# Performance work log

Measured on AMD Instinct MI355X. Metric: run time of the kernel, lower is better.

The kernel has to match this reference:

```python
import jax, jax.numpy as jnp
import numpy as np

STYLE_STRENGTH = 0.5
EPS = 1e-8


def _whiten(f):
    # f: [C, H, W] -> ZCA-whitened feature (zero mean, identity covariance)
    C = f.shape[0]
    x = f.reshape(C, -1)
    mu = x.mean(axis=1, keepdims=True)
    xc = x - mu
    cov = (xc @ xc.T) / (x.shape[1] - 1)          # [C, C]
    evals, evecs = jnp.linalg.eigh(cov)
    evals = jnp.maximum(evals, EPS)
    Wm = (evecs * (evals ** -0.5)) @ evecs.T
    return (Wm @ xc).reshape(f.shape)


def _color(f, style):
    # recolor whitened f with the covariance/mean of style. f, style: [C, H, W]
    C = f.shape[0]
    x = f.reshape(C, -1)
    s = style.reshape(C, -1)
    smu = s.mean(axis=1, keepdims=True)
    sc = s - smu
    cov = (sc @ sc.T) / (s.shape[1] - 1)
    evals, evecs = jnp.linalg.eigh(cov)
    evals = jnp.maximum(evals, EPS)
    Cm = (evecs * (evals ** 0.5)) @ evecs.T
    return (Cm @ x + smu).reshape(f.shape)


def _extract_patches3(f):
    # f: [B, C, H, W] -> [B, P, C, 3, 3], P = (H-2)*(W-2), stride 1, no padding
    B, C, H, W = f.shape
    nh, nw = H - 2, W - 2
    shifts = [f[:, :, i:i + nh, j:j + nw] for i in range(3) for j in range(3)]
    p = jnp.stack(shifts, axis=-1)                      # [B, C, nh, nw, 9]
    p = p.reshape(B, C, nh * nw, 9).transpose(0, 2, 1, 3)
    return p.reshape(B, nh * nw, C, 3, 3)


def _conv_valid(x, k):
    # x: [C, Hp, Wp], k: [O, C, kh, kw] -> [O, Hp-kh+1, Wp-kw+1]
    return jax.lax.conv_general_dilated(
        x[None], k, window_strides=(1, 1), padding='VALID',
        dimension_numbers=('NCHW', 'OIHW', 'NCHW'))[0]


def _deconv_norm(H, W, k, dtype):
    # overlap counts of k x k patches at stride 1 with centered crop (pad=(k-1)//2)
    th = jnp.arange(1, H + 1)
    tw = jnp.arange(1, W + 1)
    rh = (jnp.minimum(th, k - 1) - jnp.maximum(0, th - (H - 1)) + 1).astype(dtype)
    rw = (jnp.minimum(tw, k - 1) - jnp.maximum(0, tw - (W - 1)) + 1).astype(dtype)
    return rh[:, None] * rw[None, :]                    # [H, W]


def setup_inputs() -> dict:
    key = jax.random.key(0)
    kc, ks = jax.random.split(key)
    B, C, H, W = 4, 512, 64, 64
    return {
        'content_feature': jax.random.normal(kc, (B, C, H, W), dtype=jnp.float32),
        'style_feature': jax.random.normal(ks, (B, C, H, W), dtype=jnp.float32),
        'patch_size': 3,
        'patch_stride': 1,
    }


def reference(content_feature, style_feature, patch_size, patch_stride):
    B, C, H, W = content_feature.shape
    pad = (patch_size - 1) // 2

    # whitening of content and style features (per-sample ZCA)
    nc = jax.vmap(_whiten)(content_feature)
    ns = jax.vmap(_whiten)(style_feature)

    # style patches as conv kernels: [B, P, C, 3, 3]
    kern = _extract_patches3(ns)
    knorm = jnp.sqrt(jnp.sum(kern * kern, axis=(2, 3, 4), keepdims=True))
    kern_n = kern / knorm

    # cosine-similarity matching conv: [B, P, H, W]
    ncp = jnp.pad(nc, ((0, 0), (0, 0), (pad, pad), (pad, pad)))
    score = jax.vmap(_conv_valid)(ncp, kern_n)

    # hard argmax one-hot over patch dim
    P = kern.shape[1]
    idx = jnp.argmax(score, axis=1)                     # [B, H, W]
    onehot = jax.nn.one_hot(idx, P, dtype=score.dtype).transpose(0, 3, 1, 2)

    # transpose-conv reassembly == conv with flipped, channel-swapped kernels
    oh_pad = jnp.pad(onehot, ((0, 0), (0, 0), (pad, pad), (pad, pad)))
    kern_t = jnp.flip(kern, axis=(-2, -1)).transpose(0, 2, 1, 3, 4)  # [B, C, P, 3, 3]
    deconv = jax.vmap(_conv_valid)(oh_pad, kern_t)      # [B, C, H, W]

    reassembled = deconv / _deconv_norm(H, W, patch_size, deconv.dtype)[None, None]

    # recolor with style statistics, blend with content
    stylized = jax.vmap(_color)(reassembled, style_feature)
    return (1.0 - STYLE_STRENGTH) * content_feature + STYLE_STRENGTH * stylized
```

## Files before the change

kernel.cpp:

```cpp
#include <hip/hip_runtime.h>
#include <stdint.h>


#define C_   512
#define H_   64
#define W_   64
#define HW_  4096
#define P_   3844
#define PW_  62
#define NIT_ 10

static const long CHW_ = (long)C_ * HW_;
static const long CC_  = (long)C_ * C_;

typedef _Float16 f16x8 __attribute__((ext_vector_type(8)));
typedef float    f32x16 __attribute__((ext_vector_type(16)));

enum { GM_COV = 0, GM_NST = 1, GM_PLAIN = 2, GM_SCALE_RCP = 3, GM_NSMUL = 4, GM_NSMUL_F = 5, GM_COLOR = 6 };

template<int MODE, bool TB>
__global__ __launch_bounds__(256)
void gemm_k(const float* __restrict__ A, const float* __restrict__ Bm, float* __restrict__ Cm_,
            const float* __restrict__ sarr, const float* __restrict__ ex1, const float* __restrict__ ex2,
            int M, int N, int K, long sA, long sB, long sC, long sE1, float cscale)
{
    int z = blockIdx.z;
    const float* Ab; const float* Bb; float* Cb;
    float fs = 1.0f;
    if (MODE == GM_NSMUL || MODE == GM_NSMUL_F) {
        if (z < 8) {
            Ab = A   + (long)z * CC_;
            Bb = ex1 + (long)z * CC_;
            if (MODE == GM_NSMUL_F) fs = sqrtf(sarr[z]);
        } else {
            Ab = ex1 + (long)(z - 8) * CC_;
            Bb = Bm  + (long)(z - 8) * CC_;
            if (MODE == GM_NSMUL_F) fs = rsqrtf(sarr[z - 8]);
        }
        Cb = Cm_ + (long)z * CC_;
    } else {
        Ab = A   + (long)z * sA;
        Bb = Bm  + (long)z * sB;
        Cb = Cm_ + (long)z * sC;
        if (MODE == GM_SCALE_RCP) fs = 1.0f / sarr[z];
    }

    __shared__ float As[16][64];
    __shared__ float Bs[16][64];

    int tid = threadIdx.x;
    int tx = tid & 15, ty = tid >> 4;
    int i0 = blockIdx.x * 64;
    int j0 = blockIdx.y * 64;

    int lr = tid >> 2;
    int lk = (tid & 3) << 2;

    float acc[4][4] = {};

    for (int k0 = 0; k0 < K; k0 += 16) {
        float4 va = *(const float4*)(Ab + (long)(i0 + lr) * K + (k0 + lk));
        As[lk + 0][lr] = va.x; As[lk + 1][lr] = va.y; As[lk + 2][lr] = va.z; As[lk + 3][lr] = va.w;
        if (TB) {
            float4 vb = *(const float4*)(Bb + (long)(j0 + lr) * K + (k0 + lk));
            Bs[lk + 0][lr] = vb.x; Bs[lk + 1][lr] = vb.y; Bs[lk + 2][lr] = vb.z; Bs[lk + 3][lr] = vb.w;
        } else {
            int kr = tid >> 4, jc = (tid & 15) << 2;
            float4 vb = *(const float4*)(Bb + (long)(k0 + kr) * N + (j0 + jc));
            *(float4*)&Bs[kr][jc] = vb;
        }
        __syncthreads();
        #pragma unroll
        for (int k = 0; k < 16; ++k) {
            float4 av = *(const float4*)&As[k][ty * 4];
            float4 bv = *(const float4*)&Bs[k][tx * 4];
            acc[0][0] += av.x * bv.x; acc[0][1] += av.x * bv.y; acc[0][2] += av.x * bv.z; acc[0][3] += av.x * bv.w;
            acc[1][0] += av.y * bv.x; acc[1][1] += av.y * bv.y; acc[1][2] += av.y * bv.z; acc[1][3] += av.y * bv.w;
            acc[2][0] += av.z * bv.x; acc[2][1] += av.z * bv.y; acc[2][2] += av.z * bv.z; acc[2][3] += av.z * bv.w;
            acc[3][0] += av.w * bv.x; acc[3][1] += av.w * bv.y; acc[3][2] += av.w * bv.z; acc[3][3] += av.w * bv.w;
        }
        __syncthreads();
    }

    #pragma unroll
    for (int u = 0; u < 4; ++u) {
        int row  = i0 + ty * 4 + u;
        int col0 = j0 + tx * 4;
        float o[4];
        if (MODE == GM_COLOR) {
            const float* cv = ex1 + (long)z * sE1 + (long)row * N + col0;
            float mu = ex2[z * C_ + row];
            #pragma unroll
            for (int v = 0; v < 4; ++v) o[v] = 0.5f * cv[v] + 0.5f * (acc[u][v] + mu);
        } else {
            #pragma unroll
            for (int v = 0; v < 4; ++v) {
                if (MODE == GM_COV)      o[v] = acc[u][v] * cscale;
                else if (MODE == GM_NST) o[v] = (row == col0 + v ? 1.5f : 0.0f) - 0.5f * acc[u][v];
                else                     o[v] = acc[u][v] * fs;
            }
        }
        *(float4*)&Cb[(long)row * N + col0] = make_float4(o[0], o[1], o[2], o[3]);
    }
}

__global__ __launch_bounds__(256)
void k_center(const float* __restrict__ content, const float* __restrict__ style,
              float* __restrict__ xc, float* __restrict__ means)
{
    int bz = blockIdx.x;
    int z = bz >> 9, c = bz & 511;
    const float* src = (z < 4) ? (content + ((long)z * C_ + c) * HW_)
                               : (style   + ((long)(z - 4) * C_ + c) * HW_);
    float* dst = xc + (long)bz * HW_;
    int tid = threadIdx.x;
    float s = 0.f;
    for (int k = tid; k < HW_; k += 256) s += src[k];
    __shared__ float red[4];
    #pragma unroll
    for (int m = 32; m >= 1; m >>= 1) s += __shfl_down(s, m);
    if ((tid & 63) == 0) red[tid >> 6] = s;
    __syncthreads();
    float mean = (red[0] + red[1] + red[2] + red[3]) * (1.0f / HW_);
    for (int k = tid; k < HW_; k += 256) dst[k] = src[k] - mean;
    if (tid == 0) means[bz] = mean;
}

__global__ void k_infnorm(const float* __restrict__ cov, float* __restrict__ snorm)
{
    int z = blockIdx.x; int tid = threadIdx.x;
    const float* Mz = cov + (long)z * CC_;
    for (int r = tid; r < C_; r += 256) {
        const float4* row = (const float4*)(Mz + (long)r * C_);
        float s = 0.f;
        for (int k = 0; k < C_ / 4; ++k) {
            float4 v = row[k];
            s += fabsf(v.x) + fabsf(v.y) + fabsf(v.z) + fabsf(v.w);
        }
        atomicMax((unsigned*)&snorm[z], __float_as_uint(s));
    }
}

__global__ void k_nsinit(const float* __restrict__ cov, const float* __restrict__ snorm,
                         float* __restrict__ T, float* __restrict__ Z1)
{
    long i = (long)blockIdx.x * 256 + threadIdx.x;
    int z = (int)(i >> 18);
    long rc = i & (CC_ - 1);
    int row = (int)(rc >> 9), col = (int)(rc & 511);
    float v = -0.5f * cov[i] / snorm[z];
    if (row == col) v += 1.5f;
    T[i] = v;
    Z1[i] = v;
}

__global__ void k_q(const float* __restrict__ nsw, float* __restrict__ q)
{
    int b = blockIdx.x, y = blockIdx.y * 4 + threadIdx.y, x = threadIdx.x;
    const float* base = nsw + (long)b * CHW_ + y * W_ + x;
    float s = 0.f;
    for (int c = 0; c < C_; ++c) { float v = base[(long)c * HW_]; s += v * v; }
    q[(long)b * HW_ + y * W_ + x] = s;
}

__global__ void k_rkn(const float* __restrict__ q, float* __restrict__ rkn)
{
    int b = blockIdx.x;
    const float* qb = q + (long)b * HW_;
    for (int p = threadIdx.x; p < P_; p += 256) {
        int pu = p / PW_, pv = p % PW_;
        float s = 0.f;
        #pragma unroll
        for (int i = 0; i < 3; ++i)
            #pragma unroll
            for (int j = 0; j < 3; ++j)
                s += qb[(pu + i) * W_ + pv + j];
        rkn[b * P_ + p] = rsqrtf(fmaxf(s, 1e-20f));
    }
}

#define SC_CH 16
__global__ __launch_bounds__(256)
void k_score(const float* __restrict__ nc, const float* __restrict__ nsw,
             const float* __restrict__ rkn, unsigned long long* __restrict__ packed)
{
    int b  = blockIdx.z;
    int p0 = blockIdx.x * 256;
    int y0 = blockIdx.y;
    const float* ncb = nc  + (long)b * CHW_;
    const float* nsb = nsw + (long)b * CHW_;

    __shared__ __align__(16) _Float16 sA[2][2][3][66][8];
    __shared__ __align__(16) _Float16 sB[2][2][8][64][8];

    int tid  = threadIdx.x;
    int w    = tid >> 6;
    int lane = tid & 63;
    int l31  = lane & 31;
    int h    = lane >> 5;

    int pu0 = p0 / PW_;
    int pw0 = p0 + w * 64;

    int pn0 = pw0 + l31;
    int pn1 = pw0 + 32 + l31;
    int q0 = pn0 < P_ - 1 ? pn0 : P_ - 1;
    int q1 = pn1 < P_ - 1 ? pn1 : P_ - 1;
    int brow0 = q0 / PW_ - pu0, bcol0 = q0 % PW_;
    int brow1 = q1 / PW_ - pu0, bcol1 = q1 % PW_;

    f32x16 acc00 = {}, acc01 = {}, acc10 = {}, acc11 = {};

    for (int c0 = 0; c0 < C_; c0 += SC_CH) {
        for (int idx = tid; idx < 2 * 3 * 66; idx += 256) {
            int x = idx % 66; int gr = idx / 66;
            int r = gr % 3, g = gr / 3;
            int gy = y0 - 1 + r, gx = x - 1;
            bool ok = ((unsigned)gy < 64u) && ((unsigned)gx < 64u);
            const float* src = ncb + (long)(c0 + g * 8) * HW_ + gy * W_ + gx;
            f16x8 hi8, lo8;
            #pragma unroll
            for (int e = 0; e < 8; ++e) {
                float v = ok ? src[(long)e * HW_] : 0.f;
                _Float16 hi = (_Float16)v;
                hi8[e] = hi;
                lo8[e] = (_Float16)(v - (float)hi);
            }
            *(f16x8*)&sA[0][g][r][x][0] = hi8;
            *(f16x8*)&sA[1][g][r][x][0] = lo8;
        }
        for (int idx = tid; idx < 2 * 8 * 64; idx += 256) {
            int x = idx & 63; int gr = idx >> 6;
            int r = gr & 7, g = gr >> 3;
            int gy = pu0 + r;
            bool ok = gy < 64;
            const float* src = nsb + (long)(c0 + g * 8) * HW_ + gy * W_ + x;
            f16x8 hi8, lo8;
            #pragma unroll
            for (int e = 0; e < 8; ++e) {
                float v = ok ? src[(long)e * HW_] : 0.f;
                _Float16 hi = (_Float16)v;
                hi8[e] = hi;
                lo8[e] = (_Float16)(v - (float)hi);
            }
            *(f16x8*)&sB[0][g][r][x][0] = hi8;
            *(f16x8*)&sB[1][g][r][x][0] = lo8;
        }
        __syncthreads();

        #pragma unroll
        for (int i = 0; i < 3; ++i) {
            #pragma unroll
            for (int j = 0; j < 3; ++j) {
                f16x8 a0h = *(const f16x8*)&sA[0][h][i][l31 + j][0];
                f16x8 a0l = *(const f16x8*)&sA[1][h][i][l31 + j][0];
                f16x8 a1h = *(const f16x8*)&sA[0][h][i][32 + l31 + j][0];
                f16x8 a1l = *(const f16x8*)&sA[1][h][i][32 + l31 + j][0];
                f16x8 b0h = *(const f16x8*)&sB[0][h][brow0 + i][bcol0 + j][0];
                f16x8 b0l = *(const f16x8*)&sB[1][h][brow0 + i][bcol0 + j][0];
                f16x8 b1h = *(const f16x8*)&sB[0][h][brow1 + i][bcol1 + j][0];
                f16x8 b1l = *(const f16x8*)&sB[1][h][brow1 + i][bcol1 + j][0];

                acc00 = __builtin_amdgcn_mfma_f32_32x32x16_f16(a0l, b0h, acc00, 0, 0, 0);
                acc00 = __builtin_amdgcn_mfma_f32_32x32x16_f16(a0h, b0l, acc00, 0, 0, 0);
                acc00 = __builtin_amdgcn_mfma_f32_32x32x16_f16(a0h, b0h, acc00, 0, 0, 0);

                acc01 = __builtin_amdgcn_mfma_f32_32x32x16_f16(a0l, b1h, acc01, 0, 0, 0);
                acc01 = __builtin_amdgcn_mfma_f32_32x32x16_f16(a0h, b1l, acc01, 0, 0, 0);
                acc01 = __builtin_amdgcn_mfma_f32_32x32x16_f16(a0h, b1h, acc01, 0, 0, 0);

                acc10 = __builtin_amdgcn_mfma_f32_32x32x16_f16(a1l, b0h, acc10, 0, 0, 0);
                acc10 = __builtin_amdgcn_mfma_f32_32x32x16_f16(a1h, b0l, acc10, 0, 0, 0);
                acc10 = __builtin_amdgcn_mfma_f32_32x32x16_f16(a1h, b0h, acc10, 0, 0, 0);

                acc11 = __builtin_amdgcn_mfma_f32_32x32x16_f16(a1l, b1h, acc11, 0, 0, 0);
                acc11 = __builtin_amdgcn_mfma_f32_32x32x16_f16(a1h, b1l, acc11, 0, 0, 0);
                acc11 = __builtin_amdgcn_mfma_f32_32x32x16_f16(a1h, b1h, acc11, 0, 0, 0);
            }
        }
        __syncthreads();
    }

    bool v0 = pn0 < P_, v1 = pn1 < P_;
    float rk0 = v0 ? rkn[b * P_ + pn0] : 0.f;
    float rk1 = v1 ? rkn[b * P_ + pn1] : 0.f;

    #pragma unroll
    for (int mt = 0; mt < 2; ++mt) {
        const f32x16& A0 = mt ? acc10 : acc00;
        const f32x16& A1 = mt ? acc11 : acc01;
        #pragma unroll
        for (int r = 0; r < 16; ++r) {
            float s0 = v0 ? A0[r] * rk0 : -3.0e38f;
            float s1 = v1 ? A1[r] * rk1 : -3.0e38f;
            float best = s0; int bp = pn0;
            if (s1 > best) { best = s1; bp = pn1; }
            #pragma unroll
            for (int m = 1; m <= 16; m <<= 1) {
                float ob = __shfl_xor(best, m);
                int   op = __shfl_xor(bp, m);
                if (ob > best || (ob == best && op < bp)) { best = ob; bp = op; }
            }
            if (l31 == 0 && best > -2.9e38f) {
                int mr = (r & 3) + 8 * (r >> 2) + 4 * h;
                int px = mt * 32 + mr;
                unsigned ub = __float_as_uint(best);
                ub = (ub & 0x80000000u) ? ~ub : (ub | 0x80000000u);
                unsigned long long enc = ((unsigned long long)ub << 32) | (unsigned)(0xFFFFFFFFu - (unsigned)bp);
                atomicMax(&packed[(long)b * HW_ + y0 * W_ + px], enc);
            }
        }
    }
}

__global__ __launch_bounds__(256)
void k_reasm(const unsigned long long* __restrict__ packed, const float* __restrict__ nsw,
             float* __restrict__ reasm)
{
    int b = blockIdx.x, y = blockIdx.y;
    int x = threadIdx.x, tc = threadIdx.y;
    const float* nsb = nsw + (long)b * CHW_;
    int soff[9]; float msk[9];
    #pragma unroll
    for (int dy = -1; dy <= 1; ++dy) {
        #pragma unroll
        for (int dx = -1; dx <= 1; ++dx) {
            int k = (dy + 1) * 3 + (dx + 1);
            int u = y + dy, v = x + dx;
            if ((unsigned)u < 64u && (unsigned)v < 64u) {
                unsigned long long e = packed[(long)b * HW_ + u * W_ + v];
                int p = (int)(0xFFFFFFFFu - (unsigned)(e & 0xFFFFFFFFull));
                int pu = p / PW_, pv = p - pu * PW_;
                soff[k] = (pu + (1 - dy)) * W_ + (pv + (1 - dx));
                msk[k] = 1.f;
            } else { soff[k] = 0; msk[k] = 0.f; }
        }
    }
    int rh = (y == 0 || y == 63) ? 2 : 3;
    int rw = (x == 0 || x == 63) ? 2 : 3;
    float inv = 1.f / (float)(rh * rw);
    for (int c = tc; c < C_; c += 4) {
        const float* cb = nsb + (long)c * HW_;
        float s = 0.f;
        #pragma unroll
        for (int k = 0; k < 9; ++k) s += msk[k] * cb[soff[k]];
        reasm[((long)b * C_ + c) * HW_ + y * W_ + x] = s * inv;
    }
}

extern "C" void kernel_launch(void* const* d_in, const int* in_sizes, int n_in,
                              void* d_out, int out_size, void* d_ws, size_t ws_size,
                              hipStream_t stream)
{
    const float* content = (const float*)d_in[0];
    const float* style   = (const float*)d_in[1];
    float* out = (float*)d_out;
    float* ws  = (float*)d_ws;

    float* XC    = ws;
    float* NC    = XC    + 8 * CHW_;
    float* SLABA = NC    + 8 * CHW_;
    float* SLABB = SLABA + 16 * CC_;
    float* TBUF  = SLABB + 16 * CC_;
    float* MEANS = TBUF  + 8 * CC_;
    float* SNORM = MEANS + 4096;
    float* Q     = SNORM + 16;
    float* RKN   = Q     + 16384;
    unsigned long long* PACKED = (unsigned long long*)(RKN + 15392);

    float* COV   = SLABB;
    float* REASM = XC;

    hipMemsetAsync(SNORM, 0, 16 * sizeof(float), stream);
    hipMemsetAsync(PACKED, 0, (size_t)4 * HW_ * 8, stream);

    k_center<<<dim3(4096), dim3(256), 0, stream>>>(content, style, XC, MEANS);

    gemm_k<GM_COV, true><<<dim3(8, 8, 8), dim3(256), 0, stream>>>(
        XC, XC, COV, nullptr, nullptr, nullptr, 512, 512, 4096, CHW_, CHW_, CC_, 0, 1.0f / 4095.0f);

    k_infnorm<<<dim3(8), dim3(256), 0, stream>>>(COV, SNORM);
    k_nsinit<<<dim3(8192), dim3(256), 0, stream>>>(COV, SNORM, TBUF, SLABA + 8 * CC_);
    gemm_k<GM_SCALE_RCP, false><<<dim3(8, 8, 8), dim3(256), 0, stream>>>(
        COV, TBUF, SLABA, SNORM, nullptr, nullptr, 512, 512, 512, CC_, CC_, CC_, 0, 0.f);

    float* curS = SLABA; float* outS = SLABB;
    for (int it = 2; it <= NIT_; ++it) {
        gemm_k<GM_NST, false><<<dim3(8, 8, 8), dim3(256), 0, stream>>>(
            curS + 8 * CC_, curS, TBUF, nullptr, nullptr, nullptr, 512, 512, 512, CC_, CC_, CC_, 0, 0.f);
        if (it == NIT_)
            gemm_k<GM_NSMUL_F, false><<<dim3(8, 8, 16), dim3(256), 0, stream>>>(
                curS, curS + 8 * CC_, outS, SNORM, TBUF, nullptr, 512, 512, 512, 0, 0, 0, 0, 0.f);
        else
            gemm_k<GM_NSMUL, false><<<dim3(8, 8, 16), dim3(256), 0, stream>>>(
                curS, curS + 8 * CC_, outS, SNORM, TBUF, nullptr, 512, 512, 512, 0, 0, 0, 0, 0.f);
        float* t = curS; curS = outS; outS = t;
    }

    gemm_k<GM_PLAIN, false><<<dim3(8, 64, 8), dim3(256), 0, stream>>>(
        curS + 8 * CC_, XC, NC, nullptr, nullptr, nullptr, 512, 4096, 512, CC_, CHW_, CHW_, 0, 0.f);

    k_q<<<dim3(4, 16), dim3(64, 4), 0, stream>>>(NC + 4 * CHW_, Q);
    k_rkn<<<dim3(4), dim3(256), 0, stream>>>(Q, RKN);

    k_score<<<dim3(16, 64, 4), dim3(256), 0, stream>>>(NC, NC + 4 * CHW_, RKN, PACKED);

    k_reasm<<<dim3(4, 64), dim3(64, 4), 0, stream>>>(PACKED, NC + 4 * CHW_, REASM);

    gemm_k<GM_COLOR, false><<<dim3(8, 64, 4), dim3(256), 0, stream>>>(
        curS + 4 * CC_, REASM, out, nullptr, content, MEANS + 2048,
        512, 4096, 512, CC_, CHW_, CHW_, CHW_, 0.f);
}
```

Measured before the change: 3.656 ms.

## Move all GEMMs to split-fp16 MFMA with hi/lo operand storage

Replaces the scalar FP32 shared-memory GEMMs (covariance, Newton-Schulz iterations, whitening and coloring) with MFMA 32x32x16 fp16 kernels. Each operand is split into high and low fp16 parts, and three MFMAs per tile (hi*hi, hi*lo, lo*hi) approximate FP32 accuracy. Newton-Schulz matrices are now stored directly as hi/lo fp16 pairs, which halves the traffic for those intermediates and reorganises the workspace layout. The trade-off is extra conversion work on load and slightly reduced precision compared with true FP32.

```diff
diff --git a/kernel.cpp b/kernel.cpp
--- a/kernel.cpp
+++ b/kernel.cpp
@@ -16,91 +16,167 @@
 typedef _Float16 f16x8 __attribute__((ext_vector_type(8)));
 typedef float    f32x16 __attribute__((ext_vector_type(16)));
 
-enum { GM_COV = 0, GM_NST = 1, GM_PLAIN = 2, GM_SCALE_RCP = 3, GM_NSMUL = 4, GM_NSMUL_F = 5, GM_COLOR = 6 };
-
-template<int MODE, bool TB>
+#define SQ_NST  0
+#define SQ_MUL  1
+#define SQ_MULF 2
+#define RC_COV    0
+#define RC_WHITEN 1
+#define RC_COLOR  2
+
+template<int MODE>
 __global__ __launch_bounds__(256)
-void gemm_k(const float* __restrict__ A, const float* __restrict__ Bm, float* __restrict__ Cm_,
-            const float* __restrict__ sarr, const float* __restrict__ ex1, const float* __restrict__ ex2,
-            int M, int N, int K, long sA, long sB, long sC, long sE1, float cscale)
-{
+void gemm_sq(const _Float16* __restrict__ A1h, const _Float16* __restrict__ A1l,
+             const _Float16* __restrict__ B1h, const _Float16* __restrict__ B1l,
+             _Float16* __restrict__ D1h, _Float16* __restrict__ D1l,
+             const _Float16* __restrict__ A2h, const _Float16* __restrict__ A2l,
+             const _Float16* __restrict__ B2h, const _Float16* __restrict__ B2l,
+             _Float16* __restrict__ D2h, _Float16* __restrict__ D2l,
+             const float* __restrict__ sarr)
+{
+    int z = blockIdx.z; int zz = z & 7; bool sec = z >= 8;
+    const _Float16* Ah = (sec ? A2h : A1h) + (long)zz * CC_;
+    const _Float16* Al = (sec ? A2l : A1l) + (long)zz * CC_;
+    const _Float16* Bh = (sec ? B2h : B1h) + (long)zz * CC_;
+    const _Float16* Bl = (sec ? B2l : B1l) + (long)zz * CC_;
+    _Float16* Dh = (sec ? D2h : D1h) + (long)zz * CC_;
+    _Float16* Dl = (sec ? D2l : D1l) + (long)zz * CC_;
+    float scl = 1.0f;
+    if (MODE == SQ_MULF) scl = sec ? rsqrtf(sarr[zz]) : sqrtf(sarr[zz]);
+
+    __shared__ __align__(16) _Float16 sA[2][2][64][8];
+    __shared__ __align__(16) _Float16 sB[2][2][64][8];
+
+    int tid = threadIdx.x;
+    int w = tid >> 6, lane = tid & 63, l31 = lane & 31, h = lane >> 5;
+    int i0 = blockIdx.x * 64, j0 = blockIdx.y * 64;
+    int wm = (w >> 1) * 32, wn = (w & 1) * 32;
+
+    int spl = tid >> 7, sm = (tid >> 1) & 63, sh = tid & 1;
+    const _Float16* Asrc = spl ? Al : Ah;
+    const _Float16* Bsrc = spl ? Bl : Bh;
+
+    f32x16 acc = {};
+    for (int c0 = 0; c0 < 512; c0 += 16) {
+        *(f16x8*)&sA[spl][sh][sm][0] = *(const f16x8*)(Asrc + (long)(i0 + sm) * 512 + c0 + sh * 8);
+        *(f16x8*)&sB[spl][sh][sm][0] = *(const f16x8*)(Bsrc + (long)(j0 + sm) * 512 + c0 + sh * 8);
+        __syncthreads();
+        f16x8 ah = *(const f16x8*)&sA[0][h][wm + l31][0];
+        f16x8 al = *(const f16x8*)&sA[1][h][wm + l31][0];
+        f16x8 bh = *(const f16x8*)&sB[0][h][wn + l31][0];
+        f16x8 bl = *(const f16x8*)&sB[1][h][wn + l31][0];
+        acc = __builtin_amdgcn_mfma_f32_32x32x16_f16(al, bh, acc, 0, 0, 0);
+        acc = __builtin_amdgcn_mfma_f32_32x32x16_f16(ah, bl, acc, 0, 0, 0);
+        acc = __builtin_amdgcn_mfma_f32_32x32x16_f16(ah, bh, acc, 0, 0, 0);
+        __syncthreads();
+    }
+    #pragma unroll
+    for (int r = 0; r < 16; ++r) {
+        int row = i0 + wm + (r & 3) + 8 * (r >> 2) + 4 * h;
+        int col = j0 + wn + l31;
+        float v = acc[r];
+        if (MODE == SQ_NST) v = (row == col ? 1.5f : 0.0f) - 0.5f * v;
+        else                v *= scl;
+        _Float16 hi = (_Float16)v;
+        Dh[(long)row * 512 + col] = hi;
+        Dl[(long)row * 512 + col] = (_Float16)(v - (float)hi);
+    }
+}
+
+template<int MODE>
+__global__ __launch_bounds__(256)
+void gemm_rect(const _Float16* __restrict__ APh, const _Float16* __restrict__ APl,
+               const float* __restrict__ Asrc32, const float* __restrict__ Bsrc32,
+               float* __restrict__ Dout, const float* __restrict__ content,
+               const float* __restrict__ means)
+{
+    const int K = (MODE == RC_COV) ? 4096 : 512;
     int z = blockIdx.z;
-    const float* Ab; const float* Bb; float* Cb;
-    float fs = 1.0f;
-    if (MODE == GM_NSMUL || MODE == GM_NSMUL_F) {
-        if (z < 8) {
-            Ab = A   + (long)z * CC_;
-            Bb = ex1 + (long)z * CC_;
-            if (MODE == GM_NSMUL_F) fs = sqrtf(sarr[z]);
+    int tid = threadIdx.x;
+    int w = tid >> 6, lane = tid & 63, l31 = lane & 31, h = lane >> 5;
+    int i0 = blockIdx.x * 64, j0 = blockIdx.y * 128;
+    int wm = (w >> 1) * 32, wn = (w & 1) * 64;
+
+    __shared__ __align__(16) _Float16 sA[2][2][64][8];
+    __shared__ __align__(16) _Float16 sB[2][2][128][8];
+
+    const float* Bz = Bsrc32 + (long)z * CHW_;
+    int az = (MODE == RC_COLOR) ? z + 4 : z;
+
+    f32x16 acc0 = {}, acc1 = {};
+
+    for (int c0 = 0; c0 < K; c0 += 16) {
+        if (MODE == RC_COV) {
+            int m = tid >> 2, kq = tid & 3;
+            const float* a = Asrc32 + (long)z * CHW_ + (long)(i0 + m) * HW_ + c0 + kq * 4;
+            float4 va = *(const float4*)a;
+            _Float16 hi[4], lo[4];
+            float vv[4] = {va.x, va.y, va.z, va.w};
+            #pragma unroll
+            for (int e = 0; e < 4; ++e) { hi[e] = (_Float16)vv[e]; lo[e] = (_Float16)(vv[e] - (float)hi[e]); }
+            *(__attribute__((ext_vector_type(4))) _Float16*)&sA[0][kq >> 1][m][(kq & 1) * 4] =
+                *(__attribute__((ext_vector_type(4))) _Float16*)hi;
+            *(__attribute__((ext_vector_type(4))) _Float16*)&sA[1][kq >> 1][m][(kq & 1) * 4] =
+                *(__attribute__((ext_vector_type(4))) _Float16*)lo;
         } else {
-            Ab = ex1 + (long)(z - 8) * CC_;
-            Bb = Bm  + (long)(z - 8) * CC_;
-            if (MODE == GM_NSMUL_F) fs = rsqrtf(sarr[z - 8]);
-        }
-        Cb = Cm_ + (long)z * CC_;
-    } else {
-        Ab = A   + (long)z * sA;
-        Bb = Bm  + (long)z * sB;
-        Cb = Cm_ + (long)z * sC;
-        if (MODE == GM_SCALE_RCP) fs = 1.0f / sarr[z];
-    }
-
-    __shared__ float As[16][64];
-    __shared__ float Bs[16][64];
-
-    int tid = threadIdx.x;
-    int tx = tid & 15, ty = tid >> 4;
-    int i0 = blockIdx.x * 64;
-    int j0 = blockIdx.y * 64;
-
-    int lr = tid >> 2;
-    int lk = (tid & 3) << 2;
-
-    float acc[4][4] = {};
-
-    for (int k0 = 0; k0 < K; k0 += 16) {
-        float4 va = *(const float4*)(Ab + (long)(i0 + lr) * K + (k0 + lk));
-        As[lk + 0][lr] = va.x; As[lk + 1][lr] = va.y; As[lk + 2][lr] = va.z; As[lk + 3][lr] = va.w;
-        if (TB) {
-            float4 vb = *(const float4*)(Bb + (long)(j0 + lr) * K + (k0 + lk));
-            Bs[lk + 0][lr] = vb.x; Bs[lk + 1][lr] = vb.y; Bs[lk + 2][lr] = vb.z; Bs[lk + 3][lr] = vb.w;
+            int spl = tid >> 7, sm = (tid >> 1) & 63, sh = tid & 1;
+            const _Float16* a = (spl ? APl : APh) + (long)az * CC_ + (long)(i0 + sm) * 512 + c0 + sh * 8;
+            *(f16x8*)&sA[spl][sh][sm][0] = *(const f16x8*)a;
+        }
+        if (MODE == RC_COV) {
+            int n = tid >> 1, sh = tid & 1;
+            const float* b = Bz + (long)(j0 + n) * HW_ + c0 + sh * 8;
+            float4 v0 = *(const float4*)b, v1 = *(const float4*)(b + 4);
+            float vv[8] = {v0.x, v0.y, v0.z, v0.w, v1.x, v1.y, v1.z, v1.w};
+            f16x8 hi8, lo8;
+            #pragma unroll
+            for (int e = 0; e < 8; ++e) { _Float16 hh = (_Float16)vv[e]; hi8[e] = hh; lo8[e] = (_Float16)(vv[e] - (float)hh); }
+            *(f16x8*)&sB[0][sh][n][0] = hi8;
+            *(f16x8*)&sB[1][sh][n][0] = lo8;
         } else {
-            int kr = tid >> 4, jc = (tid & 15) << 2;
-            float4 vb = *(const float4*)(Bb + (long)(k0 + kr) * N + (j0 + jc));
-            *(float4*)&Bs[kr][jc] = vb;
+            int n = tid & 127, sh = tid >> 7;
+            const float* b = Bz + (long)(c0 + sh * 8) * HW_ + j0 + n;
+            f16x8 hi8, lo8;
+            #pragma unroll
+            for (int e = 0; e < 8; ++e) {
+                float v = b[(long)e * HW_];
+                _Float16 hh = (_Float16)v; hi8[e] = hh; lo8[e] = (_Float16)(v - (float)hh);
+            }
+            *(f16x8*)&sB[0][sh][n][0] = hi8;
+            *(f16x8*)&sB[1][sh][n][0] = lo8;
         }
         __syncthreads();
+        f16x8 ah = *(const f16x8*)&sA[0][h][wm + l31][0];
+        f16x8 al = *(const f16x8*)&sA[1][h][wm + l31][0];
+        f16x8 b0h = *(const f16x8*)&sB[0][h][wn + l31][0];
+        f16x8 b0l = *(const f16x8*)&sB[1][h][wn + l31][0];
+        f16x8 b1h = *(const f16x8*)&sB[0][h][wn + 32 + l31][0];
+        f16x8 b1l = *(const f16x8*)&sB[1][h][wn + 32 + l31][0];
+        acc0 = __builtin_amdgcn_mfma_f32_32x32x16_f16(al, b0h, acc0, 0, 0, 0);
+        acc0 = __builtin_amdgcn_mfma_f32_32x32x16_f16(ah, b0l, acc0, 0, 0, 0);
+        acc0 = __builtin_amdgcn_mfma_f32_32x32x16_f16(ah, b0h, acc0, 0, 0, 0);
+        acc1 = __builtin_amdgcn_mfma_f32_32x32x16_f16(al, b1h, acc1, 0, 0, 0);
+        acc1 = __builtin_amdgcn_mfma_f32_32x32x16_f16(ah, b1l, acc1, 0, 0, 0);
+        acc1 = __builtin_amdgcn_mfma_f32_32x32x16_f16(ah, b1h, acc1, 0, 0, 0);
+        __syncthreads();
+    }
+
+    #pragma unroll
+    for (int nt = 0; nt < 2; ++nt) {
+        const f32x16& A = nt ? acc1 : acc0;
         #pragma unroll
-        for (int k = 0; k < 16; ++k) {
-            float4 av = *(const float4*)&As[k][ty * 4];
-            float4 bv = *(const float4*)&Bs[k][tx * 4];
-            acc[0][0] += av.x * bv.x; acc[0][1] += av.x * bv.y; acc[0][2] += av.x * bv.z; acc[0][3] += av.x * bv.w;
-            acc[1][0] += av.y * bv.x; acc[1][1] += av.y * bv.y; acc[1][2] += av.y * bv.z; acc[1][3] += av.y * bv.w;
-            acc[2][0] += av.z * bv.x; acc[2][1] += av.z * bv.y; acc[2][2] += av.z * bv.z; acc[2][3] += av.z * bv.w;
-            acc[3][0] += av.w * bv.x; acc[3][1] += av.w * bv.y; acc[3][2] += av.w * bv.z; acc[3][3] += av.w * bv.w;
-        }
-        __syncthreads();
-    }
-
-    #pragma unroll
-    for (int u = 0; u < 4; ++u) {
-        int row  = i0 + ty * 4 + u;
-        int col0 = j0 + tx * 4;
-        float o[4];
-        if (MODE == GM_COLOR) {
-            const float* cv = ex1 + (long)z * sE1 + (long)row * N + col0;
-            float mu = ex2[z * C_ + row];
-            #pragma unroll
-            for (int v = 0; v < 4; ++v) o[v] = 0.5f * cv[v] + 0.5f * (acc[u][v] + mu);
-        } else {
-            #pragma unroll
-            for (int v = 0; v < 4; ++v) {
-                if (MODE == GM_COV)      o[v] = acc[u][v] * cscale;
-                else if (MODE == GM_NST) o[v] = (row == col0 + v ? 1.5f : 0.0f) - 0.5f * acc[u][v];
-                else                     o[v] = acc[u][v] * fs;
-            }
-        }
-        *(float4*)&Cb[(long)row * N + col0] = make_float4(o[0], o[1], o[2], o[3]);
+        for (int r = 0; r < 16; ++r) {
+            int row = i0 + wm + (r & 3) + 8 * (r >> 2) + 4 * h;
+            int col = j0 + wn + nt * 32 + l31;
+            if (MODE == RC_COV) {
+                Dout[(long)z * CC_ + (long)row * 512 + col] = A[r] * (1.0f / 4095.0f);
+            } else if (MODE == RC_WHITEN) {
+                Dout[(long)z * CHW_ + (long)row * HW_ + col] = A[r];
+            } else {
+                long idx = (long)z * CHW_ + (long)row * HW_ + col;
+                float mu = means[(z + 4) * C_ + row];
+                Dout[idx] = 0.5f * content[idx] + 0.5f * (A[r] + mu);
+            }
+        }
     }
 }
 
@@ -142,16 +218,19 @@
 }
 
 __global__ void k_nsinit(const float* __restrict__ cov, const float* __restrict__ snorm,
-                         float* __restrict__ T, float* __restrict__ Z1)
+                         _Float16* __restrict__ CVH, _Float16* __restrict__ CVL,
+                         _Float16* __restrict__ TH,  _Float16* __restrict__ TL,
+                         _Float16* __restrict__ ZH,  _Float16* __restrict__ ZL)
 {
     long i = (long)blockIdx.x * 256 + threadIdx.x;
     int z = (int)(i >> 18);
     long rc = i & (CC_ - 1);
     int row = (int)(rc >> 9), col = (int)(rc & 511);
-    float v = -0.5f * cov[i] / snorm[z];
-    if (row == col) v += 1.5f;
-    T[i] = v;
-    Z1[i] = v;
+    float cs = cov[i] / snorm[z];
+    float t = (row == col ? 1.5f : 0.0f) - 0.5f * cs;
+    _Float16 ch = (_Float16)cs; CVH[i] = ch; CVL[i] = (_Float16)(cs - (float)ch);
+    _Float16 th = (_Float16)t;  TH[i] = th;  TL[i] = (_Float16)(t - (float)th);
+    ZH[i] = th; ZL[i] = TL[i];
 }
 
 __global__ void k_q(const float* __restrict__ nsw, float* __restrict__ q)
@@ -355,20 +434,28 @@
     const float* content = (const float*)d_in[0];
     const float* style   = (const float*)d_in[1];
     float* out = (float*)d_out;
-    float* ws  = (float*)d_ws;
-
-    float* XC    = ws;
-    float* NC    = XC    + 8 * CHW_;
-    float* SLABA = NC    + 8 * CHW_;
-    float* SLABB = SLABA + 16 * CC_;
-    float* TBUF  = SLABB + 16 * CC_;
-    float* MEANS = TBUF  + 8 * CC_;
-    float* SNORM = MEANS + 4096;
-    float* Q     = SNORM + 16;
-    float* RKN   = Q     + 16384;
-    unsigned long long* PACKED = (unsigned long long*)(RKN + 15392);
-
-    float* COV   = SLABB;
+
+    char* base = (char*)d_ws;
+    float* XC = (float*)base;
+    float* NC = XC + 8 * CHW_;
+    char* ncb = (char*)NC;
+    float*    COV = (float*)ncb;
+    _Float16* CVH = (_Float16*)(ncb + (8 << 20));
+    _Float16* CVL = (_Float16*)(ncb + (12 << 20));
+    _Float16* TH  = (_Float16*)(ncb + (16 << 20));
+    _Float16* TL  = (_Float16*)(ncb + (20 << 20));
+    char* q = (char*)(NC + 8 * CHW_);
+    _Float16* YaH = (_Float16*)q;             _Float16* YaL = (_Float16*)(q + (4 << 20));
+    _Float16* ZaH = (_Float16*)(q + (8 << 20));  _Float16* ZaL = (_Float16*)(q + (12 << 20));
+    _Float16* YbH = (_Float16*)(q + (16 << 20)); _Float16* YbL = (_Float16*)(q + (20 << 20));
+    _Float16* ZbH = (_Float16*)(q + (24 << 20)); _Float16* ZbL = (_Float16*)(q + (28 << 20));
+    char* t = q + (32 << 20);
+    float* MEANS = (float*)t;                         t += 4096 * 4;
+    float* SNORM = (float*)t;                         t += 16 * 4;
+    float* Q     = (float*)t;                         t += 16384 * 4;
+    float* RKN   = (float*)t;                         t += 15392 * 4;
+    unsigned long long* PACKED = (unsigned long long*)t;
+
     float* REASM = XC;
 
     hipMemsetAsync(SNORM, 0, 16 * sizeof(float), stream);
@@ -376,29 +463,32 @@
 
     k_center<<<dim3(4096), dim3(256), 0, stream>>>(content, style, XC, MEANS);
 
-    gemm_k<GM_COV, true><<<dim3(8, 8, 8), dim3(256), 0, stream>>>(
-        XC, XC, COV, nullptr, nullptr, nullptr, 512, 512, 4096, CHW_, CHW_, CC_, 0, 1.0f / 4095.0f);
+    gemm_rect<RC_COV><<<dim3(8, 4, 8), dim3(256), 0, stream>>>(
+        nullptr, nullptr, XC, XC, COV, nullptr, nullptr);
 
     k_infnorm<<<dim3(8), dim3(256), 0, stream>>>(COV, SNORM);
-    k_nsinit<<<dim3(8192), dim3(256), 0, stream>>>(COV, SNORM, TBUF, SLABA + 8 * CC_);
-    gemm_k<GM_SCALE_RCP, false><<<dim3(8, 8, 8), dim3(256), 0, stream>>>(
-        COV, TBUF, SLABA, SNORM, nullptr, nullptr, 512, 512, 512, CC_, CC_, CC_, 0, 0.f);
-
-    float* curS = SLABA; float* outS = SLABB;
+    k_nsinit<<<dim3(8192), dim3(256), 0, stream>>>(COV, SNORM, CVH, CVL, TH, TL, ZaH, ZaL);
+    gemm_sq<SQ_MUL><<<dim3(8, 8, 8), dim3(256), 0, stream>>>(
+        CVH, CVL, TH, TL, YaH, YaL, CVH, CVL, TH, TL, YaH, YaL, nullptr);
+
+    _Float16 *YcH = YaH, *YcL = YaL, *ZcH = ZaH, *ZcL = ZaL;
+    _Float16 *YnH = YbH, *YnL = YbL, *ZnH = ZbH, *ZnL = ZbL;
     for (int it = 2; it <= NIT_; ++it) {
-        gemm_k<GM_NST, false><<<dim3(8, 8, 8), dim3(256), 0, stream>>>(
-            curS + 8 * CC_, curS, TBUF, nullptr, nullptr, nullptr, 512, 512, 512, CC_, CC_, CC_, 0, 0.f);
+        gemm_sq<SQ_NST><<<dim3(8, 8, 8), dim3(256), 0, stream>>>(
+            ZcH, ZcL, YcH, YcL, TH, TL, ZcH, ZcL, YcH, YcL, TH, TL, nullptr);
         if (it == NIT_)
-            gemm_k<GM_NSMUL_F, false><<<dim3(8, 8, 16), dim3(256), 0, stream>>>(
-                curS, curS + 8 * CC_, outS, SNORM, TBUF, nullptr, 512, 512, 512, 0, 0, 0, 0, 0.f);
+            gemm_sq<SQ_MULF><<<dim3(8, 8, 16), dim3(256), 0, stream>>>(
+                YcH, YcL, TH, TL, YnH, YnL, TH, TL, ZcH, ZcL, ZnH, ZnL, SNORM);
         else
-            gemm_k<GM_NSMUL, false><<<dim3(8, 8, 16), dim3(256), 0, stream>>>(
-                curS, curS + 8 * CC_, outS, SNORM, TBUF, nullptr, 512, 512, 512, 0, 0, 0, 0, 0.f);
-        float* t = curS; curS = outS; outS = t;
-    }
-
-    gemm_k<GM_PLAIN, false><<<dim3(8, 64, 8), dim3(256), 0, stream>>>(
-        curS + 8 * CC_, XC, NC, nullptr, nullptr, nullptr, 512, 4096, 512, CC_, CHW_, CHW_, 0, 0.f);
+            gemm_sq<SQ_MUL><<<dim3(8, 8, 16), dim3(256), 0, stream>>>(
+                YcH, YcL, TH, TL, YnH, YnL, TH, TL, ZcH, ZcL, ZnH, ZnL, nullptr);
+        _Float16* s;
+        s = YcH; YcH = YnH; YnH = s;  s = YcL; YcL = YnL; YnL = s;
+        s = ZcH; ZcH = ZnH; ZnH = s;  s = ZcL; ZcL = ZnL; ZnL = s;
+    }
+
+    gemm_rect<RC_WHITEN><<<dim3(8, 32, 8), dim3(256), 0, stream>>>(
+        ZcH, ZcL, nullptr, XC, NC, nullptr, nullptr);
 
     k_q<<<dim3(4, 16), dim3(64, 4), 0, stream>>>(NC + 4 * CHW_, Q);
     k_rkn<<<dim3(4), dim3(256), 0, stream>>>(Q, RKN);
@@ -407,7 +497,6 @@
 
     k_reasm<<<dim3(4, 64), dim3(64, 4), 0, stream>>>(PACKED, NC + 4 * CHW_, REASM);
 
-    gemm_k<GM_COLOR, false><<<dim3(8, 64, 4), dim3(256), 0, stream>>>(
-        curS + 4 * CC_, REASM, out, nullptr, content, MEANS + 2048,
-        512, 4096, 512, CC_, CHW_, CHW_, CHW_, 0.f);
-}
+    gemm_rect<RC_COLOR><<<dim3(8, 32, 4), dim3(256), 0, stream>>>(
+        YcH, YcL, nullptr, REASM, out, content, MEANS);
+}
```

Result: faster. 3.010 ms (-17.7%).
